# Optimization experiments

Measured on AMD Instinct MI355X. Metric: run time of the kernel, lower is better.

The kernel has to match this reference:

```python
import jax, jax.numpy as jnp
import numpy as np

N = 100000      # nodes
E = 1600000     # edges (avg degree 16)
G = 64          # graphs in batch
IN_DIM, HID, C2, C3, HEADS, NCLS = 64, 128, 64, 32, 4, 5
EPS = 1e-5
NEG_SLOPE = 0.2


def setup_inputs() -> dict:
    key = jax.random.key(0)
    ks = jax.random.split(key, 32)

    def w(k, fan_in, shape):
        return jax.random.normal(k, shape, dtype=jnp.float32) * (1.0 / np.sqrt(fan_in))

    x = jax.random.normal(ks[0], (N, IN_DIM), dtype=jnp.float32)
    edge_index = jax.random.randint(ks[1], (2, E), 0, N)
    batch = jnp.sort(jax.random.randint(ks[2], (N,), 0, G))

    inp = {"x": x, "edge_index": edge_index, "batch": batch}
    # GCN layers (PyG GCNConv: weight then symmetric-normalized aggregation, bias after)
    inp.update(W1=w(ks[3], IN_DIM, (IN_DIM, HID)), b1=jnp.zeros((HID,), jnp.float32))
    inp.update(W2=w(ks[4], HID, (HID, C2)), b2=jnp.zeros((C2,), jnp.float32))
    inp.update(W3=w(ks[5], C2, (C2, C3)), b3=jnp.zeros((C3,), jnp.float32))
    # BatchNorm (inference: running stats)
    def bn_params(k, d):
        k1, k2, k3 = jax.random.split(k, 3)
        return (1.0 + 0.1 * jax.random.normal(k1, (d,), jnp.float32),
                0.1 * jax.random.normal(k2, (d,), jnp.float32),
                0.1 * jax.random.normal(k3, (d,), jnp.float32),
                jax.random.uniform(k, (d,), jnp.float32, 0.5, 1.5))
    inp["g1"], inp["be1"], inp["m1"], inp["v1"] = bn_params(ks[6], HID)
    inp["g2"], inp["be2"], inp["m2"], inp["v2"] = bn_params(ks[7], C2)
    inp["g3"], inp["be3"], inp["m3"], inp["v3"] = bn_params(ks[8], C3)
    # GAT (heads=4, out=32, concat=False -> mean over heads)
    inp["Wg"] = w(ks[9], C3, (C3, HEADS * C3))
    inp["ag_s"] = w(ks[10], C3, (HEADS, C3))
    inp["ag_d"] = w(ks[11], C3, (HEADS, C3))
    inp["bg"] = jnp.zeros((C3,), jnp.float32)
    # classifier MLP 32 -> 16 -> 5
    inp["Wc1"] = w(ks[12], C3, (C3, 16)); inp["bc1"] = jnp.zeros((16,), jnp.float32)
    inp["Wc2"] = w(ks[13], 16, (16, NCLS)); inp["bc2"] = jnp.zeros((NCLS,), jnp.float32)
    return inp


def _bn(h, g, be, m, v):
    return (h - m) * jax.lax.rsqrt(v + EPS) * g + be


def reference(x, edge_index, batch,
              W1, b1, g1, be1, m1, v1,
              W2, b2, g2, be2, m2, v2,
              W3, b3, g3, be3, m3, v3,
              Wg, ag_s, ag_d, bg,
              Wc1, bc1, Wc2, bc2):
    n = x.shape[0]
    loop = jnp.arange(n)
    src = jnp.concatenate([edge_index[0], loop])  # add self-loops (PyG default)
    dst = jnp.concatenate([edge_index[1], loop])

    # GCN symmetric normalization: deg from dst (col), norm = d^-1/2[src]*d^-1/2[dst]
    deg = jnp.zeros((n,), x.dtype).at[dst].add(1.0)
    dinv = jax.lax.rsqrt(deg)  # deg >= 1 due to self-loops
    norm = (dinv[src] * dinv[dst])[:, None]

    def gcn(h, W, b):
        h = h @ W
        return jax.ops.segment_sum(h[src] * norm, dst, num_segments=n) + b

    h = jax.nn.relu(_bn(gcn(x, W1, b1), g1, be1, m1, v1))
    h = jax.nn.relu(_bn(gcn(h, W2, b2), g2, be2, m2, v2))
    h = jax.nn.relu(_bn(gcn(h, W3, b3), g3, be3, m3, v3))

    # GAT: per-edge attention, segment softmax over incoming edges per dst
    hh = (h @ Wg).reshape(n, HEADS, C3)          # [N,H,D]
    a_s = jnp.einsum('nhd,hd->nh', hh, ag_s)     # [N,H]
    a_d = jnp.einsum('nhd,hd->nh', hh, ag_d)
    e = jax.nn.leaky_relu(a_s[src] + a_d[dst], NEG_SLOPE)  # [Eall,H]
    emax = jax.lax.stop_gradient(jax.ops.segment_max(e, dst, num_segments=n))
    ee = jnp.exp(e - emax[dst])
    den = jax.ops.segment_sum(ee, dst, num_segments=n)
    att = ee / den[dst]                          # [Eall,H]
    agg = jax.ops.segment_sum(att[:, :, None] * hh[src], dst, num_segments=n)
    h = jax.nn.relu(agg.mean(axis=1) + bg)       # concat=False -> mean heads

    # global mean pool over graphs
    cnt = jax.ops.segment_sum(jnp.ones((n,), h.dtype), batch, num_segments=G)
    pooled = jax.ops.segment_sum(h, batch, num_segments=G) / jnp.maximum(cnt, 1.0)[:, None]

    # classifier (dropout inactive in eval)
    out = jax.nn.relu(pooled @ Wc1 + bc1) @ Wc2 + bc2
    return out
```

## Files before the change

### kernel.cpp

```cpp
#include <hip/hip_runtime.h>

#define EPSN   1e-5f
#define NEGS   0.2f
#define NGRAPH 64
#define BSHIFT 9
#define NPBK   512
#define GCAP   96
#define NPART  64
#define PSTR   (NGRAPH * 32 + NGRAPH)

typedef _Float16 half_t;
typedef _Float16 halfv8 __attribute__((ext_vector_type(8)));
typedef _Float16 halfv4 __attribute__((ext_vector_type(4)));
typedef _Float16 halfv2 __attribute__((ext_vector_type(2)));

__device__ __forceinline__ float lrelu(float e) { return e > 0.f ? e : NEGS * e; }

__global__ void k_bin_count(const int* __restrict__ ed, int* __restrict__ bsize,
                            int E, int NB) {
    __shared__ int lcnt[1024];
    for (int i = threadIdx.x; i < NB; i += 256) lcnt[i] = 0;
    __syncthreads();
    int chunk = (E + gridDim.x - 1) / gridDim.x;
    int lo = blockIdx.x * chunk;
    int hi = min(E, lo + chunk);
    for (int e = lo + threadIdx.x; e < hi; e += 256)
        atomicAdd(&lcnt[ed[e] >> BSHIFT], 1);
    __syncthreads();
    for (int b = threadIdx.x; b < NB; b += 256)
        if (lcnt[b]) atomicAdd(&bsize[b], lcnt[b]);
}
__global__ void k_bucket_scan(const int* __restrict__ bsize, int* __restrict__ bbase,
                              int* __restrict__ gcur, int NB) {
    int lane = threadIdx.x;
    if (lane >= 64) return;
    int carry = 0;
    int rounds = (NB + 63) / 64;
    for (int r = 0; r < rounds; ++r) {
        int idx = r * 64 + lane;
        int orig = (idx < NB) ? bsize[idx] : 0;
        int v = orig;
#pragma unroll
        for (int o = 1; o < 64; o <<= 1) {
            int t = __shfl_up(v, o, 64);
            if (lane >= o) v += t;
        }
        if (idx < NB) {
            int excl = carry + v - orig;
            bbase[idx] = excl;
            gcur[idx] = excl;
        }
        carry += __shfl(v, 63, 64);
    }
}
__global__ void k_bin_write(const int* __restrict__ es, const int* __restrict__ ed,
                            int* __restrict__ gcur, unsigned* __restrict__ binned,
                            int E, int NB) {
    __shared__ int lcnt[1024];
    __shared__ int lofs[1024];
    int chunk = (E + gridDim.x - 1) / gridDim.x;
    int lo = blockIdx.x * chunk;
    int hi = min(E, lo + chunk);
    for (int i = threadIdx.x; i < NB; i += 256) lcnt[i] = 0;
    __syncthreads();
    for (int e = lo + threadIdx.x; e < hi; e += 256)
        atomicAdd(&lcnt[ed[e] >> BSHIFT], 1);
    __syncthreads();
    for (int b = threadIdx.x; b < NB; b += 256) {
        int c = lcnt[b];
        lofs[b] = c ? atomicAdd(&gcur[b], c) : 0;
    }
    __syncthreads();
    for (int i = threadIdx.x; i < NB; i += 256) lcnt[i] = 0;
    __syncthreads();
    for (int e = lo + threadIdx.x; e < hi; e += 256) {
        int s = es[e], t = ed[e];
        int b = t >> BSHIFT;
        int pos = lofs[b] + atomicAdd(&lcnt[b], 1);
        binned[pos] = ((unsigned)s << BSHIFT) | (unsigned)(t & (NPBK - 1));
    }
}
__global__ void k_csr_build(const unsigned* __restrict__ binned, const int* __restrict__ bbase,
                            const int* __restrict__ bsize, int* __restrict__ rowptr,
                            int* __restrict__ deg, float* __restrict__ dinv,
                            int* __restrict__ csrc, int N) {
    __shared__ int cnt_l[NPBK];
    __shared__ int ofs_l[NPBK];
    int b = blockIdx.x;
    int base = bbase[b];
    int cnt = bsize[b];
    int nlo = b << BSHIFT;
    int nhi = min(N, nlo + NPBK);
    int nv = nhi - nlo;
    int csrbase = base + nlo;
    int tid = threadIdx.x;
    for (int i = tid; i < NPBK; i += 256) cnt_l[i] = (i < nv) ? 1 : 0;
    __syncthreads();
    for (int e = tid; e < cnt; e += 256)
        atomicAdd(&cnt_l[binned[base + e] & (NPBK - 1)], 1);
    __syncthreads();
    if (tid < 64) {
        int carry = 0;
#pragma unroll
        for (int r = 0; r < NPBK / 64; ++r) {
            int idx = r * 64 + tid;
            int orig = cnt_l[idx];
            int v = orig;
#pragma unroll
            for (int o = 1; o < 64; o <<= 1) {
                int t = __shfl_up(v, o, 64);
                if (tid >= o) v += t;
            }
            ofs_l[idx] = carry + v - orig;
            carry += __shfl(v, 63, 64);
        }
    }
    __syncthreads();
    for (int i = tid; i < nv; i += 256) {
        int node = nlo + i;
        int d = cnt_l[i];
        rowptr[node] = csrbase + ofs_l[i];
        deg[node] = d;
        dinv[node] = rsqrtf((float)d);
    }
    __syncthreads();
    for (int i = tid; i < NPBK; i += 256) cnt_l[i] = ofs_l[i];
    __syncthreads();
    for (int e = tid; e < cnt; e += 256) {
        unsigned u = binned[base + e];
        int p = atomicAdd(&cnt_l[u & (NPBK - 1)], 1);
        csrc[csrbase + p] = (int)(u >> BSHIFT);
    }
    for (int i = tid; i < nv; i += 256) {
        int p = atomicAdd(&cnt_l[i], 1);
        csrc[csrbase + p] = nlo + i;
    }
}

__global__ void k_cvt_xh(const float* __restrict__ x, const float* __restrict__ dinv,
                         half_t* __restrict__ xh, int n) {
    int total = n * 8;
    for (int q = blockIdx.x * blockDim.x + threadIdx.x; q < total;
         q += gridDim.x * blockDim.x) {
        float din = dinv[q >> 3];
        float4 a = ((const float4*)x)[q * 2];
        float4 b = ((const float4*)x)[q * 2 + 1];
        halfv8 h;
        h[0] = (half_t)(a.x * din); h[1] = (half_t)(a.y * din);
        h[2] = (half_t)(a.z * din); h[3] = (half_t)(a.w * din);
        h[4] = (half_t)(b.x * din); h[5] = (half_t)(b.y * din);
        h[6] = (half_t)(b.z * din); h[7] = (half_t)(b.w * din);
        ((halfv8*)xh)[q] = h;
    }
}

template <int K, int M, int EPI>
__global__ void k_matmulh(const half_t* __restrict__ X, const float* __restrict__ W,
                          half_t* __restrict__ Y, int n,
                          const float* __restrict__ b, const float* __restrict__ g,
                          const float* __restrict__ be, const float* __restrict__ m,
                          const float* __restrict__ v, const float* __restrict__ dinv) {
    __shared__ float Wl[K * M];
    for (int i = threadIdx.x; i < K * M / 4; i += 256)
        ((float4*)Wl)[i] = ((const float4*)W)[i];
    __syncthreads();
    const int TPR = M / 4;
    const int RPB = 256 / TPR;
    const int c4  = (threadIdx.x % TPR) * 4;
    int row = blockIdx.x * RPB + threadIdx.x / TPR;
    if (row >= n) return;
    const halfv8* xr = (const halfv8*)(X + (long long)row * K);
    float4 acc = make_float4(0.f, 0.f, 0.f, 0.f);
#pragma unroll
    for (int k8 = 0; k8 < K / 8; ++k8) {
        halfv8 xv = xr[k8];
#pragma unroll
        for (int j = 0; j < 8; ++j) {
            float xs = (float)xv[j];
            float4 wv = *(const float4*)&Wl[(k8 * 8 + j) * M + c4];
            acc.x += xs * wv.x; acc.y += xs * wv.y;
            acc.z += xs * wv.z; acc.w += xs * wv.w;
        }
    }
    if (EPI == 1) {
        float4 bb = *(const float4*)(b + c4);
        float4 mm = *(const float4*)(m + c4);
        float4 vv = *(const float4*)(v + c4);
        float4 gg = *(const float4*)(g + c4);
        float4 ee = *(const float4*)(be + c4);
        acc.x = fmaxf((acc.x + bb.x - mm.x) * rsqrtf(vv.x + EPSN) * gg.x + ee.x, 0.f);
        acc.y = fmaxf((acc.y + bb.y - mm.y) * rsqrtf(vv.y + EPSN) * gg.y + ee.y, 0.f);
        acc.z = fmaxf((acc.z + bb.z - mm.z) * rsqrtf(vv.z + EPSN) * gg.z + ee.z, 0.f);
        acc.w = fmaxf((acc.w + bb.w - mm.w) * rsqrtf(vv.w + EPSN) * gg.w + ee.w, 0.f);
    } else {
        float din = dinv[row];
        acc.x *= din; acc.y *= din; acc.z *= din; acc.w *= din;
    }
    halfv4 hv;
    hv[0] = (half_t)acc.x; hv[1] = (half_t)acc.y;
    hv[2] = (half_t)acc.z; hv[3] = (half_t)acc.w;
    *(halfv4*)(Y + (long long)row * M + c4) = hv;
}

template <int M, int EPI>
__global__ void k_agg4h(const half_t* __restrict__ A, const int* __restrict__ rowptr,
                        const int* __restrict__ deg, const int* __restrict__ csrc,
                        const float* __restrict__ dinv,
                        const float* __restrict__ b, const float* __restrict__ g,
                        const float* __restrict__ be, const float* __restrict__ m,
                        const float* __restrict__ v,
                        half_t* __restrict__ B, int n) {
    const int LPE = M / 8;
    const int EPW = 64 / LPE;
    int node = blockIdx.x * 4 + (threadIdx.x >> 6);
    if (node >= n) return;
    int lane = threadIdx.x & 63;
    int eg = lane / LPE;
    int dl = lane % LPE;
    int beg = rowptr[node];
    int end = beg + deg[node];
    float acc[8];
#pragma unroll
    for (int j = 0; j < 8; ++j) acc[j] = 0.f;
    int i = beg + eg;
    for (; i + EPW < end; i += 2 * EPW) {
        int s0 = csrc[i];
        int s1 = csrc[i + EPW];
        halfv8 x0 = *(const halfv8*)(A + (long long)s0 * M + dl * 8);
        halfv8 x1 = *(const halfv8*)(A + (long long)s1 * M + dl * 8);
#pragma unroll
        for (int j = 0; j < 8; ++j) acc[j] += (float)x0[j] + (float)x1[j];
    }
    if (i < end) {
        int s = csrc[i];
        halfv8 xv = *(const halfv8*)(A + (long long)s * M + dl * 8);
#pragma unroll
        for (int j = 0; j < 8; ++j) acc[j] += (float)xv[j];
    }
#pragma unroll
    for (int off = LPE; off < 64; off <<= 1) {
#pragma unroll
        for (int j = 0; j < 8; ++j) acc[j] += __shfl_xor(acc[j], off);
    }
    if (eg == 0) {
        float din = dinv[node];
        int d0 = dl * 8;
        float o[8];
#pragma unroll
        for (int j = 0; j < 8; ++j) o[j] = acc[j] * din;
        if (EPI == 1) {
#pragma unroll
            for (int j = 0; j < 8; ++j) {
                int d = d0 + j;
                o[j] = fmaxf((o[j] + b[d] - m[d]) * rsqrtf(v[d] + EPSN) * g[d] + be[d], 0.f);
            }
        }
        halfv8 hw;
#pragma unroll
        for (int j = 0; j < 8; ++j) hw[j] = (half_t)o[j];
        *(halfv8*)(B + (long long)node * M + d0) = hw;
    }
}

__global__ void k_wsd(const float* __restrict__ Wg, const float* __restrict__ ags,
                      const float* __restrict__ agd, float* __restrict__ wsd) {
    int j = threadIdx.x;
    if (j < 128) {
        int k = j >> 2, h = j & 3;
        float ss = 0.f, dd = 0.f;
        for (int d2 = 0; d2 < 32; ++d2) {
            float wv = Wg[k * 128 + h * 32 + d2];
            ss += wv * ags[h * 32 + d2];
            dd += wv * agd[h * 32 + d2];
        }
        wsd[j] = ss;
        wsd[128 + j] = dd;
    }
}

__global__ void k_agg_att(const half_t* __restrict__ A, const int* __restrict__ rowptr,
                          const int* __restrict__ deg, const int* __restrict__ csrc,
                          const float* __restrict__ dinv,
                          const float* __restrict__ b, const float* __restrict__ g,
                          const float* __restrict__ be, const float* __restrict__ m,
                          const float* __restrict__ v, const float* __restrict__ wsd,
                          half_t* __restrict__ H3h, float* __restrict__ a_s,
                          float* __restrict__ a_d, int n) {
    __shared__ float Wl[256];
    for (int i = threadIdx.x; i < 256; i += 256) Wl[i] = wsd[i];
    __syncthreads();
    const int M = 32, EPW = 16;
    int node = blockIdx.x * 4 + (threadIdx.x >> 6);
    if (node >= n) return;
    int lane = threadIdx.x & 63;
    int eg = lane >> 2;
    int dl = lane & 3;
    int beg = rowptr[node];
    int end = beg + deg[node];
    float acc[8];
#pragma unroll
    for (int j = 0; j < 8; ++j) acc[j] = 0.f;
    int i = beg + eg;
    for (; i + EPW < end; i += 2 * EPW) {
        int s0 = csrc[i];
        int s1 = csrc[i + EPW];
        halfv8 x0 = *(const halfv8*)(A + (long long)s0 * M + dl * 8);
        halfv8 x1 = *(const halfv8*)(A + (long long)s1 * M + dl * 8);
#pragma unroll
        for (int j = 0; j < 8; ++j) acc[j] += (float)x0[j] + (float)x1[j];
    }
    if (i < end) {
        int s = csrc[i];
        halfv8 xv = *(const halfv8*)(A + (long long)s * M + dl * 8);
#pragma unroll
        for (int j = 0; j < 8; ++j) acc[j] += (float)xv[j];
    }
#pragma unroll
    for (int off = 4; off < 64; off <<= 1) {
#pragma unroll
        for (int j = 0; j < 8; ++j) acc[j] += __shfl_xor(acc[j], off);
    }
    float din = dinv[node];
    int d0 = dl * 8;
    float hv[8];
#pragma unroll
    for (int j = 0; j < 8; ++j) {
        int d = d0 + j;
        hv[j] = fmaxf((acc[j] * din + b[d] - m[d]) * rsqrtf(v[d] + EPSN) * g[d] + be[d], 0.f);
    }
    if (eg == 0) {
        halfv8 hw;
#pragma unroll
        for (int j = 0; j < 8; ++j) hw[j] = (half_t)hv[j];
        *(halfv8*)(H3h + (long long)node * M + d0) = hw;
    }
    int h = lane & 3, sel = (lane >> 2) & 1;
    const float* wp = &Wl[sel * 128];
    float o = 0.f;
#pragma unroll
    for (int src = 0; src < 4; ++src) {
#pragma unroll
        for (int j = 0; j < 8; ++j) {
            float xv = __shfl(hv[j], src);
            o += xv * wp[(src * 8 + j) * 4 + h];
        }
    }
    if (lane < 4) a_s[node * 4 + h] = o;
    else if (lane < 8) a_d[node * 4 + h] = o;
}

__global__ void k_gat4(const half_t* __restrict__ H3h, const float* __restrict__ a_s,
                       const float* __restrict__ a_d, const int* __restrict__ rowptr,
                       const int* __restrict__ deg, const int* __restrict__ csrc,
                       const float* __restrict__ Wg, const float* __restrict__ bg,
                       const int* __restrict__ batch, float* __restrict__ pooled_part,
                       int n) {
    __shared__ float sc[4][GCAP * 4];
    __shared__ int   srcb[4][GCAP];
    __shared__ float wb[4][128];
    int w = threadIdx.x >> 6;
    int node = blockIdx.x * 4 + w;
    if (node >= n) return;
    int lane = threadIdx.x & 63;
    int beg = rowptr[node];
    int cnt = deg[node];
    bool fits = (cnt <= GCAP);
    float4 ad4 = ((const float4*)a_d)[node];
    float m0 = -1e30f, m1 = -1e30f, m2 = -1e30f, m3 = -1e30f;
    if (fits) {
        for (int e = lane; e < cnt; e += 64) {
            int s = csrc[beg + e];
            srcb[w][e] = s;
            float4 as = ((const float4*)a_s)[s];
            float e0 = lrelu(as.x + ad4.x);
            float e1 = lrelu(as.y + ad4.y);
            float e2 = lrelu(as.z + ad4.z);
            float e3 = lrelu(as.w + ad4.w);
            *(float4*)&sc[w][e * 4] = make_float4(e0, e1, e2, e3);
            m0 = fmaxf(m0, e0); m1 = fmaxf(m1, e1);
            m2 = fmaxf(m2, e2); m3 = fmaxf(m3, e3);
        }
    } else {
        for (int e = lane; e < cnt; e += 64) {
            int s = csrc[beg + e];
            float4 as = ((const float4*)a_s)[s];
            m0 = fmaxf(m0, lrelu(as.x + ad4.x));
            m1 = fmaxf(m1, lrelu(as.y + ad4.y));
            m2 = fmaxf(m2, lrelu(as.z + ad4.z));
            m3 = fmaxf(m3, lrelu(as.w + ad4.w));
        }
    }
#pragma unroll
    for (int o = 1; o < 64; o <<= 1) {
        m0 = fmaxf(m0, __shfl_xor(m0, o));
        m1 = fmaxf(m1, __shfl_xor(m1, o));
        m2 = fmaxf(m2, __shfl_xor(m2, o));
        m3 = fmaxf(m3, __shfl_xor(m3, o));
    }
    float s0 = 0.f, s1 = 0.f, s2 = 0.f, s3 = 0.f;
    if (fits) {
        for (int e = lane; e < cnt; e += 64) {
            float4 sv = *(float4*)&sc[w][e * 4];
            float p0 = __expf(sv.x - m0);
            float p1 = __expf(sv.y - m1);
            float p2 = __expf(sv.z - m2);
            float p3 = __expf(sv.w - m3);
            *(float4*)&sc[w][e * 4] = make_float4(p0, p1, p2, p3);
            s0 += p0; s1 += p1; s2 += p2; s3 += p3;
        }
    } else {
        for (int e = lane; e < cnt; e += 64) {
            int s = csrc[beg + e];
            float4 as = ((const float4*)a_s)[s];
            s0 += __expf(lrelu(as.x + ad4.x) - m0);
            s1 += __expf(lrelu(as.y + ad4.y) - m1);
            s2 += __expf(lrelu(as.z + ad4.z) - m2);
            s3 += __expf(lrelu(as.w + ad4.w) - m3);
        }
    }
#pragma unroll
    for (int o = 1; o < 64; o <<= 1) {
        s0 += __shfl_xor(s0, o);
        s1 += __shfl_xor(s1, o);
        s2 += __shfl_xor(s2, o);
        s3 += __shfl_xor(s3, o);
    }
    float inv0 = 0.25f / s0, inv1 = 0.25f / s1, inv2 = 0.25f / s2, inv3 = 0.25f / s3;
    int q = lane >> 4;
    int k = lane & 15;
    float acc[8];
#pragma unroll
    for (int j = 0; j < 8; ++j) acc[j] = 0.f;
    if (fits) {
        int i = q;
        for (; i + 4 < cnt; i += 8) {
            int sA = srcb[w][i];
            int sB = srcb[w][i + 4];
            halfv2 xA = *(const halfv2*)(H3h + (long long)sA * 32 + 2 * k);
            halfv2 xB = *(const halfv2*)(H3h + (long long)sB * 32 + 2 * k);
            float4 wA = *(float4*)&sc[w][i * 4];
            float4 wB = *(float4*)&sc[w][(i + 4) * 4];
            float a0 = (float)xA[0], a1 = (float)xA[1];
            float b0 = (float)xB[0], b1 = (float)xB[1];
            acc[0] += wA.x * a0 + wB.x * b0; acc[1] += wA.x * a1 + wB.x * b1;
            acc[2] += wA.y * a0 + wB.y * b0; acc[3] += wA.y * a1 + wB.y * b1;
            acc[4] += wA.z * a0 + wB.z * b0; acc[5] += wA.z * a1 + wB.z * b1;
            acc[6] += wA.w * a0 + wB.w * b0; acc[7] += wA.w * a1 + wB.w * b1;
        }
        if (i < cnt) {
            int s = srcb[w][i];
            halfv2 xv = *(const halfv2*)(H3h + (long long)s * 32 + 2 * k);
            float4 wv = *(float4*)&sc[w][i * 4];
            float x0 = (float)xv[0], x1 = (float)xv[1];
            acc[0] += wv.x * x0; acc[1] += wv.x * x1;
            acc[2] += wv.y * x0; acc[3] += wv.y * x1;
            acc[4] += wv.z * x0; acc[5] += wv.z * x1;
            acc[6] += wv.w * x0; acc[7] += wv.w * x1;
        }
    } else {
        for (int i = q; i < cnt; i += 4) {
            int s = csrc[beg + i];
            float4 as = ((const float4*)a_s)[s];
            float p0 = __expf(lrelu(as.x + ad4.x) - m0);
            float p1 = __expf(lrelu(as.y + ad4.y) - m1);
            float p2 = __expf(lrelu(as.z + ad4.z) - m2);
            float p3 = __expf(lrelu(as.w + ad4.w) - m3);
            halfv2 xv = *(const halfv2*)(H3h + (long long)s * 32 + 2 * k);
            float x0 = (float)xv[0], x1 = (float)xv[1];
            acc[0] += p0 * x0; acc[1] += p0 * x1;
            acc[2] += p1 * x0; acc[3] += p1 * x1;
            acc[4] += p2 * x0; acc[5] += p2 * x1;
            acc[6] += p3 * x0; acc[7] += p3 * x1;
        }
    }
#pragma unroll
    for (int o = 16; o < 64; o <<= 1) {
#pragma unroll
        for (int j = 0; j < 8; ++j) acc[j] += __shfl_xor(acc[j], o);
    }
    if (q == 0) {
        float invh[4] = {inv0, inv1, inv2, inv3};
#pragma unroll
        for (int h = 0; h < 4; ++h) {
            wb[w][h * 32 + 2 * k]     = acc[h * 2]     * invh[h];
            wb[w][h * 32 + 2 * k + 1] = acc[h * 2 + 1] * invh[h];
        }
    }
    int d = lane & 31;
    int h0 = lane >> 5;
    int half_ = h0 * 64;
    float o = 0.f;
#pragma unroll
    for (int j = 0; j < 64; ++j) {
        int jj = half_ + j;
        o += wb[w][jj] * Wg[(jj & 31) * 128 + (jj >> 5) * 32 + d];
    }
    o += __shfl_xor(o, 32);
    if (lane < 32) {
        float val = fmaxf(o + bg[d], 0.f);
        int g = batch[node];
        float* pp = pooled_part + (size_t)(blockIdx.x & (NPART - 1)) * PSTR;
        atomicAdd(&pp[g * 32 + d], val);
        if (d == 0) atomicAdd(&pp[NGRAPH * 32 + g], 1.f);
    }
}

__global__ void k_pool_reduce(const float* __restrict__ part, float* __restrict__ outp) {
    int i = blockIdx.x * blockDim.x + threadIdx.x;
    if (i >= PSTR) return;
    float s = 0.f;
#pragma unroll 8
    for (int c = 0; c < NPART; ++c) s += part[(size_t)c * PSTR + i];
    outp[i] = s;
}

__global__ void k_classifier(const float* __restrict__ pooled, const float* __restrict__ cnt,
                             const float* __restrict__ Wc1, const float* __restrict__ bc1,
                             const float* __restrict__ Wc2, const float* __restrict__ bc2,
                             float* __restrict__ out) {
    __shared__ float pl[NGRAPH * 32];
    __shared__ float t1[NGRAPH * 16];
    int tid = threadIdx.x;
    for (int i = tid; i < NGRAPH * 32; i += blockDim.x) {
        int g = i >> 5;
        pl[i] = pooled[i] / fmaxf(cnt[g], 1.f);
    }
    __syncthreads();
    for (int i = tid; i < NGRAPH * 16; i += blockDim.x) {
        int g = i >> 4, c = i & 15;
        float acc = bc1[c];
#pragma unroll
        for (int d = 0; d < 32; ++d) acc += pl[g * 32 + d] * Wc1[d * 16 + c];
        t1[i] = fmaxf(acc, 0.f);
    }
    __syncthreads();
    for (int i = tid; i < NGRAPH * 5; i += blockDim.x) {
        int g = i / 5, c = i % 5;
        float acc = bc2[c];
#pragma unroll
        for (int k = 0; k < 16; ++k) acc += t1[g * 16 + k] * Wc2[k * 5 + c];
        out[i] = acc;
    }
}

static inline dim3 gsz(long long work, int block = 256) {
    long long g = (work + block - 1) / block;
    if (g > 262144) g = 262144;
    if (g < 1) g = 1;
    return dim3((unsigned)g);
}

extern "C" void kernel_launch(void* const* d_in, const int* in_sizes, int n_in,
                              void* d_out, int out_size, void* d_ws, size_t ws_size,
                              hipStream_t stream) {
    const float* x     = (const float*)d_in[0];
    const int*   ei    = (const int*)d_in[1];
    const int*   batch = (const int*)d_in[2];
    const float* W1 = (const float*)d_in[3];  const float* b1 = (const float*)d_in[4];
    const float* W2 = (const float*)d_in[5];  const float* b2 = (const float*)d_in[6];
    const float* W3 = (const float*)d_in[7];  const float* b3 = (const float*)d_in[8];
    const float* g1 = (const float*)d_in[9];  const float* be1 = (const float*)d_in[10];
    const float* m1 = (const float*)d_in[11]; const float* v1  = (const float*)d_in[12];
    const float* g2 = (const float*)d_in[13]; const float* be2 = (const float*)d_in[14];
    const float* m2 = (const float*)d_in[15]; const float* v2  = (const float*)d_in[16];
    const float* g3 = (const float*)d_in[17]; const float* be3 = (const float*)d_in[18];
    const float* m3 = (const float*)d_in[19]; const float* v3  = (const float*)d_in[20];
    const float* Wg  = (const float*)d_in[21];
    const float* ags = (const float*)d_in[22];
    const float* agd = (const float*)d_in[23];
    const float* bg  = (const float*)d_in[24];
    const float* Wc1 = (const float*)d_in[25]; const float* bc1 = (const float*)d_in[26];
    const float* Wc2 = (const float*)d_in[27]; const float* bc2 = (const float*)d_in[28];
    float* out = (float*)d_out;

    const int N = in_sizes[0] / 64;
    const int E = in_sizes[1] / 2;
    const int* esrc = ei;
    const int* edst = ei + E;
    const int NB = (N + NPBK - 1) >> BSHIFT;

    size_t off = 0;
    auto take = [&](size_t bytes) -> void* {
        void* p = (char*)d_ws + off;
        off += bytes;
        off = (off + 255) & ~(size_t)255;
        return p;
    };
    int*    deg    = (int*)take((size_t)N * 4);
    float*  dinv   = (float*)take((size_t)N * 4);
    int*    rowptr = (int*)take((size_t)N * 4);
    int*    bsize  = (int*)take((size_t)1024 * 4);
    int*    bbase  = (int*)take((size_t)1024 * 4);
    int*    gcur   = (int*)take((size_t)1024 * 4);
    float*  wsd    = (float*)take((size_t)256 * 4);
    int*    csrc   = (int*)take((size_t)(E + N) * 4);
    half_t* bufAh  = (half_t*)take((size_t)N * 64 * 2);
    half_t* bufBh  = (half_t*)take((size_t)N * 64 * 2);
    float*  bufC   = (float*)take((size_t)N * 128 * 4);
    half_t* h3h    = (half_t*)take((size_t)N * 32 * 2);
    float*  a_s    = (float*)take((size_t)N * 4 * 4);
    float*  a_d    = (float*)take((size_t)N * 4 * 4);
    float*  ppart  = (float*)take((size_t)NPART * PSTR * 4);
    float*  pooled = (float*)take((size_t)PSTR * 4);
    float*  cnt    = pooled + NGRAPH * 32;
    unsigned* binned = (unsigned*)bufC;
    half_t* H1h    = (half_t*)bufC;
    (void)ws_size; (void)n_in; (void)out_size;

    const dim3 B256(256);

    hipMemsetAsync(bsize, 0, (size_t)NB * 4, stream);
    hipMemsetAsync(ppart, 0, (size_t)NPART * PSTR * 4, stream);
    hipLaunchKernelGGL(k_bin_count, dim3(512), B256, 0, stream, edst, bsize, E, NB);
    hipLaunchKernelGGL(k_bucket_scan, dim3(1), dim3(64), 0, stream, bsize, bbase, gcur, NB);
    hipLaunchKernelGGL(k_bin_write, dim3(512), B256, 0, stream, esrc, edst, gcur, binned, E, NB);
    hipLaunchKernelGGL(k_csr_build, dim3(NB), B256, 0, stream,
                       binned, bbase, bsize, rowptr, deg, dinv, csrc, N);
    hipLaunchKernelGGL(k_wsd, dim3(1), dim3(128), 0, stream, Wg, ags, agd, wsd);

    hipLaunchKernelGGL(k_cvt_xh, gsz((long long)N * 8), B256, 0, stream, x, dinv, bufAh, N);
    hipLaunchKernelGGL((k_agg4h<64, 0>), dim3((N + 3) / 4), B256, 0, stream,
                       bufAh, rowptr, deg, csrc, dinv,
                       nullptr, nullptr, nullptr, nullptr, nullptr, bufBh, N);
    hipLaunchKernelGGL((k_matmulh<64, 128, 1>), dim3((N + 7) / 8), B256, 0, stream,
                       bufBh, W1, H1h, N, b1, g1, be1, m1, v1, nullptr);
    hipLaunchKernelGGL((k_matmulh<128, 64, 2>), dim3((N + 15) / 16), B256, 0, stream,
                       H1h, W2, bufAh, N, nullptr, nullptr, nullptr, nullptr, nullptr, dinv);
    hipLaunchKernelGGL((k_agg4h<64, 1>), dim3((N + 3) / 4), B256, 0, stream,
                       bufAh, rowptr, deg, csrc, dinv, b2, g2, be2, m2, v2, bufBh, N);
    hipLaunchKernelGGL((k_matmulh<64, 32, 2>), dim3((N + 31) / 32), B256, 0, stream,
                       bufBh, W3, bufAh, N, nullptr, nullptr, nullptr, nullptr, nullptr, dinv);
    hipLaunchKernelGGL(k_agg_att, dim3((N + 3) / 4), B256, 0, stream,
                       bufAh, rowptr, deg, csrc, dinv, b3, g3, be3, m3, v3,
                       wsd, h3h, a_s, a_d, N);

    hipLaunchKernelGGL(k_gat4, dim3((N + 3) / 4), B256, 0, stream,
                       h3h, a_s, a_d, rowptr, deg, csrc, Wg, bg, batch, ppart, N);

    hipLaunchKernelGGL(k_pool_reduce, dim3((PSTR + 255) / 256), B256, 0, stream, ppart, pooled);
    hipLaunchKernelGGL(k_classifier, dim3(1), B256, 0, stream, pooled, cnt, Wc1, bc1, Wc2, bc2, out);
}
```

Baseline: 572.1 us.

## Fuse layer-3 aggregation with W3 matmul and reuse per-block bin counts

Adds a kernel that aggregates layer-2 features per node, applies bias, BN and ReLU, then multiplies by W3 held in shared memory. This replaces a separate aggregation kernel and matmul kernel, removing a full intermediate feature write and read plus one launch. The binning pass now saves per-block bucket counts from the counting kernel, so the write kernel no longer re-reads destinations and recounts them. The GAT aggregation loop is unrolled from two to four edges per step to raise memory-level parallelism. The costs are a 2 MB count buffer, a per-node serial 64-step dot product inside one wavefront, and higher register pressure in the GAT loop.

Result: slower. 590.7 us (+3.3%).

```diff
diff --git a/kernel.cpp b/kernel.cpp
--- a/kernel.cpp
+++ b/kernel.cpp
@@ -8,6 +8,7 @@
 #define GCAP   96
 #define NPART  64
 #define PSTR   (NGRAPH * 32 + NGRAPH)
+#define BINBLK 512
 
 typedef _Float16 half_t;
 typedef _Float16 halfv8 __attribute__((ext_vector_type(8)));
@@ -17,7 +18,7 @@
 __device__ __forceinline__ float lrelu(float e) { return e > 0.f ? e : NEGS * e; }
 
 __global__ void k_bin_count(const int* __restrict__ ed, int* __restrict__ bsize,
-                            int E, int NB) {
+                            int* __restrict__ bcnt, int E, int NB) {
     __shared__ int lcnt[1024];
     for (int i = threadIdx.x; i < NB; i += 256) lcnt[i] = 0;
     __syncthreads();
@@ -27,8 +28,11 @@
     for (int e = lo + threadIdx.x; e < hi; e += 256)
         atomicAdd(&lcnt[ed[e] >> BSHIFT], 1);
     __syncthreads();
-    for (int b = threadIdx.x; b < NB; b += 256)
-        if (lcnt[b]) atomicAdd(&bsize[b], lcnt[b]);
+    for (int b = threadIdx.x; b < NB; b += 256) {
+        int c = lcnt[b];
+        if (c) atomicAdd(&bsize[b], c);
+        bcnt[blockIdx.x * 1024 + b] = c;
+    }
 }
 __global__ void k_bucket_scan(const int* __restrict__ bsize, int* __restrict__ bbase,
                               int* __restrict__ gcur, int NB) {
@@ -54,24 +58,18 @@
     }
 }
 __global__ void k_bin_write(const int* __restrict__ es, const int* __restrict__ ed,
-                            int* __restrict__ gcur, unsigned* __restrict__ binned,
-                            int E, int NB) {
+                            const int* __restrict__ bcnt, int* __restrict__ gcur,
+                            unsigned* __restrict__ binned, int E, int NB) {
     __shared__ int lcnt[1024];
     __shared__ int lofs[1024];
     int chunk = (E + gridDim.x - 1) / gridDim.x;
     int lo = blockIdx.x * chunk;
     int hi = min(E, lo + chunk);
-    for (int i = threadIdx.x; i < NB; i += 256) lcnt[i] = 0;
-    __syncthreads();
-    for (int e = lo + threadIdx.x; e < hi; e += 256)
-        atomicAdd(&lcnt[ed[e] >> BSHIFT], 1);
-    __syncthreads();
     for (int b = threadIdx.x; b < NB; b += 256) {
-        int c = lcnt[b];
+        int c = bcnt[blockIdx.x * 1024 + b];
         lofs[b] = c ? atomicAdd(&gcur[b], c) : 0;
-    }
-    __syncthreads();
-    for (int i = threadIdx.x; i < NB; i += 256) lcnt[i] = 0;
+        lcnt[b] = 0;
+    }
     __syncthreads();
     for (int e = lo + threadIdx.x; e < hi; e += 256) {
         int s = es[e], t = ed[e];
@@ -260,6 +258,69 @@
         for (int j = 0; j < 8; ++j) hw[j] = (half_t)o[j];
         *(halfv8*)(B + (long long)node * M + d0) = hw;
     }
+}
+
+__global__ void k_agg_mm3(const half_t* __restrict__ A, const int* __restrict__ rowptr,
+                          const int* __restrict__ deg, const int* __restrict__ csrc,
+                          const float* __restrict__ dinv,
+                          const float* __restrict__ b, const float* __restrict__ g,
+                          const float* __restrict__ be, const float* __restrict__ m,
+                          const float* __restrict__ v, const float* __restrict__ W3,
+                          half_t* __restrict__ A3h, int n) {
+    __shared__ float W3l[64 * 32];
+    __shared__ float h2buf[4][64];
+    for (int i = threadIdx.x; i < 64 * 32 / 4; i += 256)
+        ((float4*)W3l)[i] = ((const float4*)W3)[i];
+    __syncthreads();
+    const int M = 64, LPE = 8, EPW = 8;
+    int w = threadIdx.x >> 6;
+    int node = blockIdx.x * 4 + w;
+    if (node >= n) return;
+    int lane = threadIdx.x & 63;
+    int eg = lane / LPE;
+    int dl = lane % LPE;
+    int beg = rowptr[node];
+    int end = beg + deg[node];
+    float acc[8];
+#pragma unroll
+    for (int j = 0; j < 8; ++j) acc[j] = 0.f;
+    int i = beg + eg;
+    for (; i + EPW < end; i += 2 * EPW) {
+        int s0 = csrc[i];
+        int s1 = csrc[i + EPW];
+        halfv8 x0 = *(const halfv8*)(A + (long long)s0 * M + dl * 8);
+        halfv8 x1 = *(const halfv8*)(A + (long long)s1 * M + dl * 8);
+#pragma unroll
+        for (int j = 0; j < 8; ++j) acc[j] += (float)x0[j] + (float)x1[j];
+    }
+    if (i < end) {
+        int s = csrc[i];
+        halfv8 xv = *(const halfv8*)(A + (long long)s * M + dl * 8);
+#pragma unroll
+        for (int j = 0; j < 8; ++j) acc[j] += (float)xv[j];
+    }
+#pragma unroll
+    for (int off = LPE; off < 64; off <<= 1) {
+#pragma unroll
+        for (int j = 0; j < 8; ++j) acc[j] += __shfl_xor(acc[j], off);
+    }
+    float din = dinv[node];
+    int d0 = dl * 8;
+    if (eg == 0) {
+#pragma unroll
+        for (int j = 0; j < 8; ++j) {
+            int d = d0 + j;
+            float h2 = fmaxf((acc[j] * din + b[d] - m[d]) * rsqrtf(v[d] + EPSN) * g[d] + be[d], 0.f);
+            h2buf[w][d] = h2;
+        }
+    }
+    int jcol = lane & 31;
+    float o = 0.f;
+#pragma unroll
+    for (int k = 0; k < 64; ++k)
+        o += h2buf[w][k] * W3l[k * 32 + jcol];
+    if (lane < 32)
+        A3h[(long long)node * 32 + jcol] = (half_t)(o * din);
 }
 
 __global__ void k_wsd(const float* __restrict__ Wg, const float* __restrict__ ags,
@@ -433,21 +494,31 @@
     for (int j = 0; j < 8; ++j) acc[j] = 0.f;
     if (fits) {
         int i = q;
-        for (; i + 4 < cnt; i += 8) {
-            int sA = srcb[w][i];
-            int sB = srcb[w][i + 4];
+        for (; i + 12 < cnt; i += 16) {
+            int sA = srcb[w][i],     sB = srcb[w][i + 4];
+            int sC = srcb[w][i + 8], sD = srcb[w][i + 12];
             halfv2 xA = *(const halfv2*)(H3h + (long long)sA * 32 + 2 * k);
             halfv2 xB = *(const halfv2*)(H3h + (long long)sB * 32 + 2 * k);
+            halfv2 xC = *(const halfv2*)(H3h + (long long)sC * 32 + 2 * k);
+            halfv2 xD = *(const halfv2*)(H3h + (long long)sD * 32 + 2 * k);
             float4 wA = *(float4*)&sc[w][i * 4];
             float4 wB = *(float4*)&sc[w][(i + 4) * 4];
+            float4 wC = *(float4*)&sc[w][(i + 8) * 4];
+            float4 wD = *(float4*)&sc[w][(i + 12) * 4];
             float a0 = (float)xA[0], a1 = (float)xA[1];
             float b0 = (float)xB[0], b1 = (float)xB[1];
-            acc[0] += wA.x * a0 + wB.x * b0; acc[1] += wA.x * a1 + wB.x * b1;
-            acc[2] += wA.y * a0 + wB.y * b0; acc[3] += wA.y * a1 + wB.y * b1;
-            acc[4] += wA.z * a0 + wB.z * b0; acc[5] += wA.z * a1 + wB.z * b1;
-            acc[6] += wA.w * a0 + wB.w * b0; acc[7] += wA.w * a1 + wB.w * b1;
-        }
-        if (i < cnt) {
+            float c0 = (float)xC[0], c1 = (float)xC[1];
+            float d0 = (float)xD[0], d1 = (float)xD[1];
+            acc[0] += wA.x * a0 + wB.x * b0 + wC.x * c0 + wD.x * d0;
+            acc[1] += wA.x * a1 + wB.x * b1 + wC.x * c1 + wD.x * d1;
+            acc[2] += wA.y * a0 + wB.y * b0 + wC.y * c0 + wD.y * d0;
+            acc[3] += wA.y * a1 + wB.y * b1 + wC.y * c1 + wD.y * d1;
+            acc[4] += wA.z * a0 + wB.z * b0 + wC.z * c0 + wD.z * d0;
+            acc[5] += wA.z * a1 + wB.z * b1 + wC.z * c1 + wD.z * d1;
+            acc[6] += wA.w * a0 + wB.w * b0 + wC.w * c0 + wD.w * d0;
+            acc[7] += wA.w * a1 + wB.w * b1 + wC.w * c1 + wD.w * d1;
+        }
+        for (; i < cnt; i += 4) {
             int s = srcb[w][i];
             halfv2 xv = *(const halfv2*)(H3h + (long long)s * 32 + 2 * k);
             float4 wv = *(float4*)&sc[w][i * 4];
@@ -593,6 +664,7 @@
     int*    bbase  = (int*)take((size_t)1024 * 4);
     int*    gcur   = (int*)take((size_t)1024 * 4);
     float*  wsd    = (float*)take((size_t)256 * 4);
+    int*    bcnt   = (int*)take((size_t)BINBLK * 1024 * 4);
     int*    csrc   = (int*)take((size_t)(E + N) * 4);
     half_t* bufAh  = (half_t*)take((size_t)N * 64 * 2);
     half_t* bufBh  = (half_t*)take((size_t)N * 64 * 2);
@@ -611,9 +683,9 @@
 
     hipMemsetAsync(bsize, 0, (size_t)NB * 4, stream);
     hipMemsetAsync(ppart, 0, (size_t)NPART * PSTR * 4, stream);
-    hipLaunchKernelGGL(k_bin_count, dim3(512), B256, 0, stream, edst, bsize, E, NB);
+    hipLaunchKernelGGL(k_bin_count, dim3(BINBLK), B256, 0, stream, edst, bsize, bcnt, E, NB);
     hipLaunchKernelGGL(k_bucket_scan, dim3(1), dim3(64), 0, stream, bsize, bbase, gcur, NB);
-    hipLaunchKernelGGL(k_bin_write, dim3(512), B256, 0, stream, esrc, edst, gcur, binned, E, NB);
+    hipLaunchKernelGGL(k_bin_write, dim3(BINBLK), B256, 0, stream, esrc, edst, bcnt, gcur, binned, E, NB);
     hipLaunchKernelGGL(k_csr_build, dim3(NB), B256, 0, stream,
                        binned, bbase, bsize, rowptr, deg, dinv, csrc, N);
     hipLaunchKernelGGL(k_wsd, dim3(1), dim3(128), 0, stream, Wg, ags, agd, wsd);
@@ -626,12 +698,10 @@
                        bufBh, W1, H1h, N, b1, g1, be1, m1, v1, nullptr);
     hipLaunchKernelGGL((k_matmulh<128, 64, 2>), dim3((N + 15) / 16), B256, 0, stream,
                        H1h, W2, bufAh, N, nullptr, nullptr, nullptr, nullptr, nullptr, dinv);
-    hipLaunchKernelGGL((k_agg4h<64, 1>), dim3((N + 3) / 4), B256, 0, stream,
-                       bufAh, rowptr, deg, csrc, dinv, b2, g2, be2, m2, v2, bufBh, N);
-    hipLaunchKernelGGL((k_matmulh<64, 32, 2>), dim3((N + 31) / 32), B256, 0, stream,
-                       bufBh, W3, bufAh, N, nullptr, nullptr, nullptr, nullptr, nullptr, dinv);
+    hipLaunchKernelGGL(k_agg_mm3, dim3((N + 3) / 4), B256, 0, stream,
+                       bufAh, rowptr, deg, csrc, dinv, b2, g2, be2, m2, v2, W3, bufBh, N);
     hipLaunchKernelGGL(k_agg_att, dim3((N + 3) / 4), B256, 0, stream,
-                       bufAh, rowptr, deg, csrc, dinv, b3, g3, be3, m3, v3,
+                       bufBh, rowptr, deg, csrc, dinv, b3, g3, be3, m3, v3,
                        wsd, h3h, a_s, a_d, N);
 
     hipLaunchKernelGGL(k_gat4, dim3((N + 3) / 4), B256, 0, stream,
```
